# Performance work log

Measured on AMD Instinct MI355X. Metric: run time of the kernel, lower is better.

## Reference

```python
import jax, jax.numpy as jnp
import numpy as np

# Quantization constants (from init_kwargs)
INPUT_SCALE = 0.05
OUTPUT_SCALE = 0.1
OUTPUT_ZERO_POINT = 0
FEATURE_BITWIDTH = 8
Q_MIN = -(1 << (FEATURE_BITWIDTH - 1))       # -128
Q_MAX = (1 << (FEATURE_BITWIDTH - 1)) - 1    #  127

B, IN_F, OUT_F = 8192, 4096, 4096


def setup_inputs() -> dict:
    key = jax.random.key(0)
    k_x, k_w, k_b, k_s = jax.random.split(key, 4)
    # int8 quantized activations and weights
    x = jax.random.randint(k_x, (B, IN_F), Q_MIN, Q_MAX + 1, dtype=jnp.int8)
    weight = jax.random.randint(k_w, (OUT_F, IN_F), Q_MIN, Q_MAX + 1, dtype=jnp.int8)
    # shifted quantized bias (int32)
    bias = jax.random.randint(k_b, (OUT_F,), -1000, 1000, dtype=jnp.int32)
    # per-output-channel weight scale (positive floats)
    weight_scale = jax.random.uniform(k_s, (OUT_F,), dtype=jnp.float32, minval=0.001, maxval=0.01)
    return {"x": x, "weight": weight, "bias": bias, "weight_scale": weight_scale}


def reference(x, weight, bias, weight_scale):
    # int32-accumulated GEMM: [B, in] @ [in, out] + bias -> [B, out]
    acc = jnp.matmul(x.astype(jnp.int32), weight.astype(jnp.int32).T,
                     preferred_element_type=jnp.int32) + bias[None, :]
    # dequant/requant epilogue with per-channel scale
    out = acc.astype(jnp.float32) * (INPUT_SCALE * weight_scale[None, :] / OUTPUT_SCALE) + OUTPUT_ZERO_POINT
    out = jnp.clip(jnp.round(out), Q_MIN, Q_MAX).astype(jnp.int8)
    return out
```

## Files before the change

### kernel.cpp

```cpp
#include <hip/hip_runtime.h>
#include <cstdint>
#include <cstddef>

#define M_DIM 8192
#define N_DIM 4096
#define K_DIM 4096

#define BM 256
#define BN 256

using i32x4 = __attribute__((ext_vector_type(4))) int;

__device__ __forceinline__ void async_load16(const void* g, void* l) {
    __builtin_amdgcn_global_load_lds(
        (const __attribute__((address_space(1))) void*)g,
        (__attribute__((address_space(3))) void*)l,
        16, 0, 0);
}

__global__ __launch_bounds__(256) void pack_i8_kernel(const int4* __restrict__ xsrc,
                                                      int* __restrict__ xdst,
                                                      const int4* __restrict__ wsrc,
                                                      int* __restrict__ wdst,
                                                      int nxblocks) {
    const bool isw = (int)blockIdx.x >= nxblocks;
    const int4* src = isw ? wsrc : xsrc;
    int*       dst  = isw ? wdst : xdst;
    const long bb   = isw ? ((long)blockIdx.x - nxblocks) : (long)blockIdx.x;
    const long base = bb * 1024 + threadIdx.x;
#pragma unroll
    for (int j = 0; j < 4; ++j) {
        const long i = base + 256 * j;
        const int4 v = src[i];
        dst[i] = (v.x & 0xff) | ((v.y & 0xff) << 8) | ((v.z & 0xff) << 16) | (v.w << 24);
    }
}

__global__ __launch_bounds__(512, 2) void qgemm_i8_kernel(const int8_t* __restrict__ A,
                                                          const int8_t* __restrict__ B,
                                                          const int* __restrict__ bias,
                                                          const float* __restrict__ wscale,
                                                          int* __restrict__ C) {
    __shared__ int8_t LDS[131072];

    const int tid  = threadIdx.x;
    const int wave = tid >> 6;
    const int lane = tid & 63;
    const int wm = wave >> 2;
    const int wn = wave & 3;
    const int bm = blockIdx.y;
    const int bn = blockIdx.x;

    const int8_t* Ab = A + (size_t)bm * BM * K_DIM;
    const int8_t* Bb = B + (size_t)bn * BN * K_DIM;

    const int l8 = lane >> 3;
    const int l7 = lane & 7;
    const int8_t* Ag = Ab + (size_t)(wave * 16 + l8) * K_DIM + ((l7 ^ l8) * 16);
    const int8_t* Bg = Bb + (size_t)(wave * 16 + l8) * K_DIM + ((l7 ^ l8) * 16);
    const int sdst = wave * 2048;

    const int l15 = lane & 15;
    const int qh  = lane >> 4;
    const int a_off0 = wm * 8192 + l15 * 128 + ((qh ^ l7) * 16);
    const int a_off1 = a_off0 ^ 64;
    const int b_off0 = 65536 + wn * 4096 + l15 * 128 + ((qh ^ l7) * 16);
    const int b_off1 = b_off0 ^ 64;

    i32x4 acc[4][4][2] = {};

#define ISSUE_HT(GB, REG, BUF, HH, T) do { \
    async_load16((GB) + (size_t)((HH) * 128)     * K_DIM + (size_t)(T) * 128, \
                 &LDS[(REG) + (BUF) * 32768 + (HH) * 16384 + sdst]); \
    async_load16((GB) + (size_t)((HH) * 128 + 8) * K_DIM + (size_t)(T) * 128, \
                 &LDS[(REG) + (BUF) * 32768 + (HH) * 16384 + sdst + 1024]); \
} while (0)

#define PHASE(BUF, MH, NH, QD, ISSUES, CHK) do { \
    i32x4 af[4][2]; i32x4 bf[2][2]; \
    _Pragma("unroll") \
    for (int mi = 0; mi < 4; ++mi) { \
        af[mi][0] = *(const i32x4*)&LDS[a_off0 + (BUF) * 32768 + (MH) * 16384 + mi * 2048]; \
        af[mi][1] = *(const i32x4*)&LDS[a_off1 + (BUF) * 32768 + (MH) * 16384 + mi * 2048]; \
    } \
    _Pragma("unroll") \
    for (int ni = 0; ni < 2; ++ni) { \
        bf[ni][0] = *(const i32x4*)&LDS[b_off0 + (BUF) * 32768 + (NH) * 16384 + ni * 2048]; \
        bf[ni][1] = *(const i32x4*)&LDS[b_off1 + (BUF) * 32768 + (NH) * 16384 + ni * 2048]; \
    } \
    ISSUES; \
    CHK; \
    __builtin_amdgcn_s_barrier(); \
    asm volatile("s_waitcnt lgkmcnt(0)" ::: "memory"); \
    __builtin_amdgcn_sched_barrier(0); \
    __builtin_amdgcn_s_setprio(1); \
    _Pragma("unroll") \
    for (int mi = 0; mi < 4; ++mi) { \
        _Pragma("unroll") \
        for (int ni = 0; ni < 2; ++ni) { \
            acc[QD][mi][ni] = __builtin_amdgcn_mfma_i32_16x16x64_i8(af[mi][0], bf[ni][0], acc[QD][mi][ni], 0, 0, 0); \
            acc[QD][mi][ni] = __builtin_amdgcn_mfma_i32_16x16x64_i8(af[mi][1], bf[ni][1], acc[QD][mi][ni], 0, 0, 0); \
        } \
    } \
    __builtin_amdgcn_s_setprio(0); \
    __builtin_amdgcn_s_barrier(); \
} while (0)

    ISSUE_HT(Bg, 65536, 0, 0, 0);
    ISSUE_HT(Ag, 0,     0, 1, 0);
    ISSUE_HT(Ag, 0,     0, 0, 0);
    ISSUE_HT(Bg, 65536, 0, 1, 0);
    ISSUE_HT(Bg, 65536, 1, 0, 1);
    ISSUE_HT(Ag, 0,     1, 1, 1);
    asm volatile("s_waitcnt vmcnt(4)" ::: "memory");
    __builtin_amdgcn_s_barrier();

    for (int i = 0; i < 16; ++i) {
        const int V = 2 * i + 1;
        const int W = 2 * i + 2;
        const int X = 2 * i + 3;
        const bool more = (i < 15);

        PHASE(0, 0, 0, 0, { ISSUE_HT(Ag, 0,     1, 0, V); }, {});
        PHASE(0, 1, 0, 1, { ISSUE_HT(Bg, 65536, 1, 1, V); }, {});
        PHASE(0, 1, 1, 2, { if (more) ISSUE_HT(Bg, 65536, 0, 0, W); }, {});
        PHASE(0, 0, 1, 3, { if (more) ISSUE_HT(Ag, 0,     0, 1, W); },
              { if (more) { asm volatile("s_waitcnt vmcnt(4)" ::: "memory"); }
                else      { asm volatile("s_waitcnt vmcnt(0)" ::: "memory"); } });
        PHASE(1, 0, 0, 0, { if (more) ISSUE_HT(Ag, 0,     0, 0, W); }, {});
        PHASE(1, 1, 0, 1, { if (more) ISSUE_HT(Bg, 65536, 0, 1, W); }, {});
        PHASE(1, 1, 1, 2, { if (more) ISSUE_HT(Bg, 65536, 1, 0, X); }, {});
        PHASE(1, 0, 1, 3, { if (more) ISSUE_HT(Ag, 0,     1, 1, X); },
              { if (more) { asm volatile("s_waitcnt vmcnt(4)" ::: "memory"); } });
    }

#undef PHASE
#undef ISSUE_HT

    const int col16 = lane & 15;
    const int rquad = (lane >> 4) * 4;
#pragma unroll
    for (int qd = 0; qd < 4; ++qd) {
        const int mh = (qd & 1) ^ (qd >> 1);
        const int nh = qd >> 1;
#pragma unroll
        for (int ni = 0; ni < 2; ++ni) {
            const int col = bn * BN + nh * 128 + wn * 32 + ni * 16 + col16;
            float s = 0.05f * wscale[col];
            s = s / 0.1f;
            const float bz = (float)bias[col];
#pragma unroll
            for (int mi = 0; mi < 4; ++mi) {
                const int row0 = bm * BM + mh * 128 + wm * 64 + mi * 16 + rquad;
#pragma unroll
                for (int r = 0; r < 4; ++r) {
                    float v = ((float)acc[qd][mi][ni][r] + bz) * s;
                    v = rintf(v);
                    v = fminf(fmaxf(v, -128.0f), 127.0f);
                    C[(size_t)(row0 + r) * N_DIM + col] = (int)v;
                }
            }
        }
    }
}

extern "C" void kernel_launch(void* const* d_in, const int* in_sizes, int n_in,
                              void* d_out, int out_size, void* d_ws, size_t ws_size,
                              hipStream_t stream) {
    const int*   x32    = (const int*)d_in[0];
    const int*   w32    = (const int*)d_in[1];
    const int*   bias   = (const int*)d_in[2];
    const float* wscale = (const float*)d_in[3];
    int*         out    = (int*)d_out;

    int8_t* xp = (int8_t*)d_ws;
    int8_t* wp = xp + (size_t)M_DIM * K_DIM;

    {
        const int nxblocks = (int)((long)M_DIM * K_DIM / 4 / 1024);
        const int nwblocks = (int)((long)N_DIM * K_DIM / 4 / 1024);
        pack_i8_kernel<<<nxblocks + nwblocks, 256, 0, stream>>>(
            (const int4*)x32, (int*)xp, (const int4*)w32, (int*)wp, nxblocks);
    }

    dim3 grid(N_DIM / BN, M_DIM / BM);
    qgemm_i8_kernel<<<grid, 512, 0, stream>>>(xp, wp, bias, wscale, out);
}
```

Baseline: 407.4 us.

## Reuse A/B LDS fragments across phases and deepen async load pipeline

Hoists the A and B register fragments out of each phase so that only the changed half (A or B) is reloaded from LDS per quadrant. This traverses quadrants in a snake order, which cuts LDS read traffic per phase. The global-to-LDS prefetch schedule is reordered so each phase waits with vmcnt(6) instead of every fourth phase with vmcnt(4), keeping more loads in flight. The risks are more live registers and a tighter dependency ordering between the issued tiles and their consumers.

```diff
diff --git a/kernel.cpp b/kernel.cpp
--- a/kernel.cpp
+++ b/kernel.cpp
@@ -68,6 +68,8 @@
     const int b_off1 = b_off0 ^ 64;
 
     i32x4 acc[4][4][2] = {};
+    i32x4 af[4][2];
+    i32x4 bf[2][2];
 
 #define ISSUE_HT(GB, REG, BUF, HH, T) do { \
     async_load16((GB) + (size_t)((HH) * 128)     * K_DIM + (size_t)(T) * 128, \
@@ -76,18 +78,27 @@
                  &LDS[(REG) + (BUF) * 32768 + (HH) * 16384 + sdst + 1024]); \
 } while (0)
 
-#define PHASE(BUF, MH, NH, QD, ISSUES, CHK) do { \
-    i32x4 af[4][2]; i32x4 bf[2][2]; \
+#define LOAD_AF(BUF, MH) do { \
     _Pragma("unroll") \
     for (int mi = 0; mi < 4; ++mi) { \
         af[mi][0] = *(const i32x4*)&LDS[a_off0 + (BUF) * 32768 + (MH) * 16384 + mi * 2048]; \
         af[mi][1] = *(const i32x4*)&LDS[a_off1 + (BUF) * 32768 + (MH) * 16384 + mi * 2048]; \
     } \
+} while (0)
+
+#define LOAD_BF(BUF, NH) do { \
     _Pragma("unroll") \
     for (int ni = 0; ni < 2; ++ni) { \
         bf[ni][0] = *(const i32x4*)&LDS[b_off0 + (BUF) * 32768 + (NH) * 16384 + ni * 2048]; \
         bf[ni][1] = *(const i32x4*)&LDS[b_off1 + (BUF) * 32768 + (NH) * 16384 + ni * 2048]; \
     } \
+} while (0)
+
+#define VM6 asm volatile("s_waitcnt vmcnt(6)" ::: "memory")
+#define VM0 asm volatile("s_waitcnt vmcnt(0)" ::: "memory")
+
+#define PHASE(LOADS, QD, ISSUES, CHK) do { \
+    LOADS; \
     ISSUES; \
     CHK; \
     __builtin_amdgcn_s_barrier(); \
@@ -106,13 +117,14 @@
     __builtin_amdgcn_s_barrier(); \
 } while (0)
 
+    ISSUE_HT(Ag, 0,     0, 0, 0);
     ISSUE_HT(Bg, 65536, 0, 0, 0);
+    ISSUE_HT(Bg, 65536, 0, 1, 0);
     ISSUE_HT(Ag, 0,     0, 1, 0);
-    ISSUE_HT(Ag, 0,     0, 0, 0);
-    ISSUE_HT(Bg, 65536, 0, 1, 0);
-    ISSUE_HT(Bg, 65536, 1, 0, 1);
+    ISSUE_HT(Ag, 0,     1, 0, 1);
+    ISSUE_HT(Bg, 65536, 1, 1, 1);
     ISSUE_HT(Ag, 0,     1, 1, 1);
-    asm volatile("s_waitcnt vmcnt(4)" ::: "memory");
+    asm volatile("s_waitcnt vmcnt(10)" ::: "memory");
     __builtin_amdgcn_s_barrier();
 
     for (int i = 0; i < 16; ++i) {
@@ -121,28 +133,38 @@
         const int X = 2 * i + 3;
         const bool more = (i < 15);
 
-        PHASE(0, 0, 0, 0, { ISSUE_HT(Ag, 0,     1, 0, V); }, {});
-        PHASE(0, 1, 0, 1, { ISSUE_HT(Bg, 65536, 1, 1, V); }, {});
-        PHASE(0, 1, 1, 2, { if (more) ISSUE_HT(Bg, 65536, 0, 0, W); }, {});
-        PHASE(0, 0, 1, 3, { if (more) ISSUE_HT(Ag, 0,     0, 1, W); },
-              { if (more) { asm volatile("s_waitcnt vmcnt(4)" ::: "memory"); }
-                else      { asm volatile("s_waitcnt vmcnt(0)" ::: "memory"); } });
-        PHASE(1, 0, 0, 0, { if (more) ISSUE_HT(Ag, 0,     0, 0, W); }, {});
-        PHASE(1, 1, 0, 1, { if (more) ISSUE_HT(Bg, 65536, 0, 1, W); }, {});
-        PHASE(1, 1, 1, 2, { if (more) ISSUE_HT(Bg, 65536, 1, 0, X); }, {});
-        PHASE(1, 0, 1, 3, { if (more) ISSUE_HT(Ag, 0,     1, 1, X); },
-              { if (more) { asm volatile("s_waitcnt vmcnt(4)" ::: "memory"); } });
+        PHASE({ LOAD_AF(0, 0); LOAD_BF(0, 0); }, 0,
+              { ISSUE_HT(Bg, 65536, 1, 0, V); }, VM6);
+        PHASE({ LOAD_BF(0, 1); }, 1,
+              { if (more) ISSUE_HT(Ag, 0,     0, 0, W); }, VM6);
+        PHASE({ LOAD_AF(0, 1); }, 2,
+              { if (more) ISSUE_HT(Bg, 65536, 0, 1, W); }, VM6);
+        PHASE({ LOAD_BF(0, 0); }, 3,
+              { if (more) ISSUE_HT(Ag, 0,     0, 1, W); },
+              { if (more) { VM6; } else { VM0; } });
+        PHASE({ LOAD_AF(1, 0); LOAD_BF(1, 0); }, 0,
+              { if (more) ISSUE_HT(Bg, 65536, 0, 0, W); }, VM6);
+        PHASE({ LOAD_BF(1, 1); }, 1,
+              { if (more) ISSUE_HT(Ag, 0,     1, 0, X); }, VM6);
+        PHASE({ LOAD_AF(1, 1); }, 2,
+              { if (more) ISSUE_HT(Bg, 65536, 1, 1, X); }, VM6);
+        PHASE({ LOAD_BF(1, 0); }, 3,
+              { if (more) ISSUE_HT(Ag, 0,     1, 1, X); }, VM6);
     }
 
 #undef PHASE
+#undef VM0
+#undef VM6
+#undef LOAD_BF
+#undef LOAD_AF
 #undef ISSUE_HT
 
     const int col16 = lane & 15;
     const int rquad = (lane >> 4) * 4;
 #pragma unroll
     for (int qd = 0; qd < 4; ++qd) {
-        const int mh = (qd & 1) ^ (qd >> 1);
-        const int nh = qd >> 1;
+        const int mh = qd >> 1;
+        const int nh = (qd >> 1) ^ (qd & 1);
 #pragma unroll
         for (int ni = 0; ni < 2; ++ni) {
             const int col = bn * BN + nh * 128 + wn * 32 + ni * 16 + col16;
```

New measurement: 389.7 us. -4.3%, faster.
